# Kernel tuning notes

Measured on AMD Instinct MI355X. Metric: run time of the kernel, lower is better.

## Reference

```python
import jax, jax.numpy as jnp
import numpy as np

S, B, NC, IMG = 7, 2, 20, 448
GRID = IMG // S  # 64 px per cell
COORD_W, NOOBJ_W = 5.0, 0.5
N_BATCH, N_GT = 16384, 20


def _left_top():
    # ltp[i, j] = (GRID * j, GRID * i)  -- x from column, y from row
    col = (jnp.arange(S) * GRID).astype(jnp.float32)
    X, Y = jnp.meshgrid(col, col, indexing='xy')
    return jnp.stack([X, Y], -1)  # [S, S, 2]


def _corners(center_xy, wh):
    half = wh * 0.5
    x1y1 = jnp.clip(center_xy - half, 0.0, IMG - 1.0)
    x2y2 = jnp.clip(center_xy + half, 0.0, IMG - 1.0)
    return jnp.concatenate([x1y1, x2y2], -1)


def _encode(groundTruth, groundLabels):
    # Vectorized objMaskAndEncoder: replaces nested python scatter loops.
    N, G, _ = groundTruth.shape
    x1, y1, x2, y2 = (groundTruth[..., k] for k in range(4))
    w, h = x2 - x1, y2 - y1
    x, y = x1 + w * 0.5, y1 + h * 0.5
    cellX = jnp.floor(x / GRID).astype(jnp.int32)
    cellY = jnp.floor(y / GRID).astype(jnp.int32)
    offset = jnp.stack([(x - cellX * GRID) / GRID,
                        (y - cellY * GRID) / GRID,
                        w / IMG, h / IMG], -1)  # [N, G, 4]
    b_idx = jnp.broadcast_to(jnp.arange(N)[:, None], (N, G))
    flat = cellY * S + cellX  # [N, G] flat cell id
    j_idx = jnp.broadcast_to(jnp.arange(G, dtype=jnp.int32)[None, :], (N, G))
    last = jnp.full((N, S * S), -1, jnp.int32).at[b_idx, flat].max(j_idx)
    gi = jnp.maximum(last, 0)
    gathered = jnp.take_along_axis(offset, gi[:, :, None], axis=1)  # [N, S*S, 4]
    gtOrd = jnp.where((last >= 0)[:, :, None], gathered, 0.0).reshape(N, S, S, 4)
    # every GT sets its class bit in its cell (not just the last one)
    gtLabels = jnp.zeros((N, S, S, NC), jnp.float32).at[
        b_idx, cellY, cellX, groundLabels].set(1.0)
    objMask = (gtLabels.sum(-1) != 0).astype(jnp.float32)
    return objMask, gtOrd, gtLabels


def _best_iou(objMask, gtOrd, preBoxes):
    N = preBoxes.shape[0]
    ltp = _left_top()
    pb = preBoxes.reshape(N, S, S, B, 4)
    pboxes = _corners(pb[..., :2] * GRID + ltp[None, :, :, None, :],
                      pb[..., 2:] * IMG)  # [N, S, S, B, 4]
    gboxes = _corners(gtOrd[..., :2] * GRID + ltp[None, :, :, :],
                      gtOrd[..., 2:] * IMG)[:, :, :, None, :]  # [N, S, S, 1, 4]
    lt = jnp.maximum(pboxes[..., :2], gboxes[..., :2])
    rb = jnp.minimum(pboxes[..., 2:], gboxes[..., 2:])
    wh = jnp.maximum(rb - lt, 0.0)
    inter = wh[..., 0] * wh[..., 1]
    a1 = (pboxes[..., 2] - pboxes[..., 0]) * (pboxes[..., 3] - pboxes[..., 1])
    a2 = (gboxes[..., 2] - gboxes[..., 0]) * (gboxes[..., 3] - gboxes[..., 1])
    iou = inter / (a1 + a2 - inter + 1e-4)  # [N, S, S, B]
    best = jnp.argmax(iou, axis=-1)
    boxObjMask = jax.nn.one_hot(best, B, dtype=jnp.float32) * objMask[..., None]
    boxIouMax = jnp.max(iou, axis=-1, keepdims=True) * boxObjMask
    return boxObjMask, boxIouMax


def _yolo_loss(preConfidence, preBoxes, preCondClasses, groundTruth, groundLabels):
    objMask, gtOrd, gtLabels = _encode(groundTruth, groundLabels)
    boxObjMask, _ = _best_iou(objMask, gtOrd, preBoxes)
    objMask, gtOrd, gtLabels, boxObjMask = map(
        jax.lax.stop_gradient, (objMask, gtOrd, gtLabels, boxObjMask))  # torch no_grad
    pb = preBoxes.reshape(-1, S, S, B, 4)
    m = boxObjMask[..., None]
    xy, wh = pb[..., :2], jnp.sqrt(pb[..., 2:])
    xyGt = gtOrd[..., None, :2]
    whGt = jnp.sqrt(gtOrd[..., None, 2:])
    coordLoss = ((jnp.square(xy - xyGt) * m).sum()
                 + (jnp.square(wh - whGt) * m).sum()) * COORD_W
    diff2 = jnp.square(preConfidence - boxObjMask)
    objLoss = (diff2 * boxObjMask).sum()
    noObjLoss = NOOBJ_W * (diff2 * (1.0 - boxObjMask)).sum()
    clsLoss = (jnp.square(preCondClasses - gtLabels).sum(-1) * objMask).sum()
    return coordLoss, objLoss, noObjLoss, clsLoss


def setup_inputs() -> dict:
    key = jax.random.key(0)
    k1, k2, k3, k4, k5, k6 = jax.random.split(key, 6)
    preConfidence = jax.random.uniform(k1, (N_BATCH, S, S, B), jnp.float32)
    preBoxes = jax.random.uniform(k2, (N_BATCH, S, S, B * 4), jnp.float32)
    preCondClasses = jax.random.uniform(k3, (N_BATCH, S, S, NC), jnp.float32)
    # realistic GT corner boxes inside the 448x448 image
    cxy = jax.random.uniform(k4, (N_BATCH, N_GT, 2), jnp.float32, 0.0, float(IMG))
    wh = jax.random.uniform(k5, (N_BATCH, N_GT, 2), jnp.float32, 10.0, 120.0)
    x1y1 = jnp.clip(cxy - wh / 2, 0.0, IMG - 1.0)
    x2y2 = jnp.clip(cxy + wh / 2, 0.0, IMG - 1.0)
    groundTruth = jnp.concatenate([x1y1, x2y2], -1)
    groundLabels = jax.random.randint(k6, (N_BATCH, N_GT), 0, NC)
    return {"preConfidence": preConfidence, "preBoxes": preBoxes,
            "preCondClasses": preCondClasses, "groundTruth": groundTruth,
            "groundLabels": groundLabels}


def reference(preConfidence, preBoxes, preCondClasses, groundTruth, groundLabels):
    return _yolo_loss(preConfidence, preBoxes, preCondClasses, groundTruth, groundLabels)
```

## Files before the change

### kernel.cpp

```cpp
#include <hip/hip_runtime.h>
#include <math.h>


#define S7 7
#define NCELL 49
#define NGT 20
#define NCLS 20
#define BPB 4
#define BPW 2
#define THREADS 256
#define NBLK 2048

__device__ __forceinline__ float clip447(float v) {
    return fminf(fmaxf(v, 0.0f), 447.0f);
}

__device__ __forceinline__ float iou_one(float4 pb, float ltx, float lty,
                                         float g1x, float g1y, float g2x, float g2y,
                                         float ga) {
    float cx = pb.x * 64.0f + ltx, cy = pb.y * 64.0f + lty;
    float w  = pb.z * 448.0f,      h  = pb.w * 448.0f;
    float p1x = clip447(cx - w * 0.5f), p1y = clip447(cy - h * 0.5f);
    float p2x = clip447(cx + w * 0.5f), p2y = clip447(cy + h * 0.5f);
    float lx = fmaxf(p1x, g1x), ly = fmaxf(p1y, g1y);
    float rx = fminf(p2x, g2x), ry = fminf(p2y, g2y);
    float iw = fmaxf(rx - lx, 0.0f), ih = fmaxf(ry - ly, 0.0f);
    float inter = iw * ih;
    float a1 = (p2x - p1x) * (p2y - p1y);
    return inter / (a1 + ga - inter + 0.0001f);
}

__global__ __launch_bounds__(THREADS) void yolo_loss_kernel(
    const float* __restrict__ preConf,
    const float* __restrict__ preBoxes,
    const float* __restrict__ preCls,
    const float* __restrict__ gtBox,
    const int*   __restrict__ gtLab,
    float* __restrict__ ws)
{
    __shared__ int      s_last[BPB][NCELL];
    __shared__ unsigned s_bits[BPB][NCELL];
    __shared__ float    s_off[BPB][NGT][4];
    __shared__ float    s_red[BPB][4];

    const int wave = threadIdx.x >> 6;
    const int lane = threadIdx.x & 63;

    float coordL = 0.0f, objL = 0.0f, noobjL = 0.0f, clsL = 0.0f;

    for (int it = 0; it < BPW; ++it) {
        const int n = it * (NBLK * BPB) + blockIdx.x * BPB + wave;

        if (lane < NCELL) {
            s_last[wave][lane] = -1;
            s_bits[wave][lane] = 0u;
        }
        __syncthreads();

        if (lane < NGT) {
            float4 g = reinterpret_cast<const float4*>(gtBox)[(size_t)n * NGT + lane];
            int lab = gtLab[(size_t)n * NGT + lane];
            float w = g.z - g.x, h = g.w - g.y;
            float x = g.x + w * 0.5f, y = g.y + h * 0.5f;
            int cx = (int)floorf(x * 0.015625f);
            int cy = (int)floorf(y * 0.015625f);
            cx = max(0, min(cx, 6));
            cy = max(0, min(cy, 6));
            int flat = cy * S7 + cx;
            s_off[wave][lane][0] = (x - (float)cx * 64.0f) * 0.015625f;
            s_off[wave][lane][1] = (y - (float)cy * 64.0f) * 0.015625f;
            s_off[wave][lane][2] = w * (1.0f / 448.0f);
            s_off[wave][lane][3] = h * (1.0f / 448.0f);
            atomicMax(&s_last[wave][flat], lane);
            atomicOr(&s_bits[wave][flat], 1u << lab);
        }
        __syncthreads();

        if (lane < NCELL) {
            const int c = lane;
            const int row = c / S7, col = c - row * S7;
            const float ltx = (float)col * 64.0f, lty = (float)row * 64.0f;

            float2 cf = reinterpret_cast<const float2*>(preConf)[(size_t)n * NCELL + c];
            int last = s_last[wave][c];
            if (last >= 0) {
                const float4* pbp = reinterpret_cast<const float4*>(preBoxes)
                                    + (size_t)n * NCELL * 2 + (size_t)c * 2;
                float4 b0 = pbp[0];
                float4 b1 = pbp[1];

                float gx = s_off[wave][last][0], gy = s_off[wave][last][1];
                float gw = s_off[wave][last][2], gh = s_off[wave][last][3];
                float gcx = gx * 64.0f + ltx, gcy = gy * 64.0f + lty;
                float gW = gw * 448.0f, gH = gh * 448.0f;
                float g1x = clip447(gcx - gW * 0.5f), g1y = clip447(gcy - gH * 0.5f);
                float g2x = clip447(gcx + gW * 0.5f), g2y = clip447(gcy + gH * 0.5f);
                float ga = (g2x - g1x) * (g2y - g1y);

                float iou0 = iou_one(b0, ltx, lty, g1x, g1y, g2x, g2y, ga);
                float iou1 = iou_one(b1, ltx, lty, g1x, g1y, g2x, g2y, ga);
                int best = (iou1 > iou0) ? 1 : 0;
                float4 pb = best ? b1 : b0;
                float confB = best ? cf.y : cf.x;
                float confO = best ? cf.x : cf.y;

                float dx = pb.x - gx, dy = pb.y - gy;
                float dw = sqrtf(pb.z) - sqrtf(gw);
                float dh = sqrtf(pb.w) - sqrtf(gh);
                coordL += dx * dx + dy * dy + dw * dw + dh * dh;
                float d = confB - 1.0f;
                objL += d * d;
                noobjL += confO * confO;
            } else {
                noobjL += cf.x * cf.x + cf.y * cf.y;
            }
        }

        {
            const float4* base4 = reinterpret_cast<const float4*>(
                preCls + (size_t)n * (NCELL * NCLS));
            #pragma unroll
            for (int t = 0; t < 4; ++t) {
                const int i = lane + t * 64;
                if (i < 245) {
                    const int e = i * 4;
                    const int c0 = e / NCLS;
                    const int k0 = e - c0 * NCLS;
                    const unsigned b0 = s_bits[wave][c0];
                    const bool cross = (k0 > NCLS - 4);
                    const unsigned b1 = cross ? s_bits[wave][c0 + 1] : b0;
                    if (b0 | b1) {
                        float4 v = base4[i];
                        float vv[4] = {v.x, v.y, v.z, v.w};
                        #pragma unroll
                        for (int j = 0; j < 4; ++j) {
                            int kj = k0 + j;
                            unsigned bb = (kj < NCLS) ? b0 : b1;
                            int kk = (kj < NCLS) ? kj : kj - NCLS;
                            if (bb) {
                                float d = vv[j] - (float)((bb >> kk) & 1u);
                                clsL += d * d;
                            }
                        }
                    }
                }
            }
        }
        __syncthreads();
    }

    for (int off = 32; off > 0; off >>= 1) {
        coordL += __shfl_down(coordL, off);
        objL   += __shfl_down(objL, off);
        noobjL += __shfl_down(noobjL, off);
        clsL   += __shfl_down(clsL, off);
    }
    if (lane == 0) {
        s_red[wave][0] = coordL;
        s_red[wave][1] = objL;
        s_red[wave][2] = noobjL;
        s_red[wave][3] = clsL;
    }
    __syncthreads();

    if (threadIdx.x == 0) {
        float c0 = 0.f, c1 = 0.f, c2 = 0.f, c3 = 0.f;
        for (int w = 0; w < BPB; ++w) {
            c0 += s_red[w][0];
            c1 += s_red[w][1];
            c2 += s_red[w][2];
            c3 += s_red[w][3];
        }
        ws[0 * NBLK + blockIdx.x] = c0 * 5.0f;
        ws[1 * NBLK + blockIdx.x] = c1;
        ws[2 * NBLK + blockIdx.x] = c2 * 0.5f;
        ws[3 * NBLK + blockIdx.x] = c3;
    }
}

__global__ __launch_bounds__(256) void reduce_kernel(
    const float* __restrict__ ws, float* __restrict__ out)
{
    const int wave = threadIdx.x >> 6;
    const int lane = threadIdx.x & 63;
    const float* src = ws + wave * NBLK;
    float s = 0.0f;
    for (int i = lane; i < NBLK; i += 64) s += src[i];
    for (int off = 32; off > 0; off >>= 1) s += __shfl_down(s, off);
    if (lane == 0) out[wave] = s;
}

extern "C" void kernel_launch(void* const* d_in, const int* in_sizes, int n_in,
                              void* d_out, int out_size, void* d_ws, size_t ws_size,
                              hipStream_t stream) {
    const float* preConf  = (const float*)d_in[0];
    const float* preBoxes = (const float*)d_in[1];
    const float* preCls   = (const float*)d_in[2];
    const float* gtBox    = (const float*)d_in[3];
    const int*   gtLab    = (const int*)d_in[4];
    float* out = (float*)d_out;
    float* ws  = (float*)d_ws;

    yolo_loss_kernel<<<NBLK, THREADS, 0, stream>>>(
        preConf, preBoxes, preCls, gtBox, gtLab, ws);
    reduce_kernel<<<1, 256, 0, stream>>>(ws, out);
}
```

Before: 134.8 us.

## Replace shared-memory atomic encoding with wave shuffles and drop block barriers

Ground-truth cell assignment and class bitmasks are now computed per wave with a shuffle loop over the 20 GT lanes, replacing shared-memory atomics. This removes all __syncthreads and the shared arrays. The class-loss loop is simplified because each float4 always falls inside a single cell, and a ballot mask lets whole empty cells be skipped. A launch-bounds occupancy hint is added, and the cell-index clamp is dropped, which relies on GT centres staying inside the image.

```diff
diff --git a/kernel.cpp b/kernel.cpp
--- a/kernel.cpp
+++ b/kernel.cpp
@@ -30,7 +30,7 @@
     return inter / (a1 + ga - inter + 0.0001f);
 }
 
-__global__ __launch_bounds__(THREADS) void yolo_loss_kernel(
+__global__ __launch_bounds__(THREADS, 8) void yolo_loss_kernel(
     const float* __restrict__ preConf,
     const float* __restrict__ preBoxes,
     const float* __restrict__ preCls,
@@ -38,10 +38,7 @@
     const int*   __restrict__ gtLab,
     float* __restrict__ ws)
 {
-    __shared__ int      s_last[BPB][NCELL];
-    __shared__ unsigned s_bits[BPB][NCELL];
-    __shared__ float    s_off[BPB][NGT][4];
-    __shared__ float    s_red[BPB][4];
+    __shared__ float s_red[BPB][4];
 
     const int wave = threadIdx.x >> 6;
     const int lane = threadIdx.x & 63;
@@ -51,46 +48,49 @@
     for (int it = 0; it < BPW; ++it) {
         const int n = it * (NBLK * BPB) + blockIdx.x * BPB + wave;
 
-        if (lane < NCELL) {
-            s_last[wave][lane] = -1;
-            s_bits[wave][lane] = 0u;
-        }
-        __syncthreads();
-
+        float offx = 0.f, offy = 0.f, offw = 0.f, offh = 0.f;
+        int flatv = 0, lab = 0;
         if (lane < NGT) {
             float4 g = reinterpret_cast<const float4*>(gtBox)[(size_t)n * NGT + lane];
-            int lab = gtLab[(size_t)n * NGT + lane];
+            lab = gtLab[(size_t)n * NGT + lane];
             float w = g.z - g.x, h = g.w - g.y;
-            float x = g.x + w * 0.5f, y = g.y + h * 0.5f;
+            float x = g.x + 0.5f * w, y = g.y + 0.5f * h;
             int cx = (int)floorf(x * 0.015625f);
             int cy = (int)floorf(y * 0.015625f);
-            cx = max(0, min(cx, 6));
-            cy = max(0, min(cy, 6));
-            int flat = cy * S7 + cx;
-            s_off[wave][lane][0] = (x - (float)cx * 64.0f) * 0.015625f;
-            s_off[wave][lane][1] = (y - (float)cy * 64.0f) * 0.015625f;
-            s_off[wave][lane][2] = w * (1.0f / 448.0f);
-            s_off[wave][lane][3] = h * (1.0f / 448.0f);
-            atomicMax(&s_last[wave][flat], lane);
-            atomicOr(&s_bits[wave][flat], 1u << lab);
+            flatv = cy * S7 + cx;
+            offx = (x - (float)cx * 64.0f) * 0.015625f;
+            offy = (y - (float)cy * 64.0f) * 0.015625f;
+            offw = w * (1.0f / 448.0f);
+            offh = h * (1.0f / 448.0f);
         }
-        __syncthreads();
+
+        int last = -1;
+        unsigned bits = 0u;
+        #pragma unroll
+        for (int j = 0; j < NGT; ++j) {
+            int fj = __shfl(flatv, j);
+            int lj = __shfl(lab, j);
+            if (fj == lane) { last = j; bits |= (1u << lj); }
+        }
+        const unsigned long long ball = __ballot(bits != 0u);
+
+        const int srcl = (last < 0) ? 0 : last;
+        const float gx = __shfl(offx, srcl);
+        const float gy = __shfl(offy, srcl);
+        const float gw = __shfl(offw, srcl);
+        const float gh = __shfl(offh, srcl);
 
         if (lane < NCELL) {
-            const int c = lane;
-            const int row = c / S7, col = c - row * S7;
+            const int row = lane / S7, col = lane - row * S7;
             const float ltx = (float)col * 64.0f, lty = (float)row * 64.0f;
 
-            float2 cf = reinterpret_cast<const float2*>(preConf)[(size_t)n * NCELL + c];
-            int last = s_last[wave][c];
+            float2 cf = reinterpret_cast<const float2*>(preConf)[(size_t)n * NCELL + lane];
             if (last >= 0) {
                 const float4* pbp = reinterpret_cast<const float4*>(preBoxes)
-                                    + (size_t)n * NCELL * 2 + (size_t)c * 2;
+                                    + (size_t)n * NCELL * 2 + (size_t)lane * 2;
                 float4 b0 = pbp[0];
                 float4 b1 = pbp[1];
 
-                float gx = s_off[wave][last][0], gy = s_off[wave][last][1];
-                float gw = s_off[wave][last][2], gh = s_off[wave][last][3];
                 float gcx = gx * 64.0f + ltx, gcy = gy * 64.0f + lty;
                 float gW = gw * 448.0f, gH = gh * 448.0f;
                 float g1x = clip447(gcx - gW * 0.5f), g1y = clip447(gcy - gH * 0.5f);
@@ -123,30 +123,20 @@
             for (int t = 0; t < 4; ++t) {
                 const int i = lane + t * 64;
                 if (i < 245) {
-                    const int e = i * 4;
-                    const int c0 = e / NCLS;
-                    const int k0 = e - c0 * NCLS;
-                    const unsigned b0 = s_bits[wave][c0];
-                    const bool cross = (k0 > NCLS - 4);
-                    const unsigned b1 = cross ? s_bits[wave][c0 + 1] : b0;
-                    if (b0 | b1) {
+                    const int c0 = i / 5;
+                    const int k0 = (i - c0 * 5) * 4;
+                    if ((ball >> c0) & 1ull) {
+                        const unsigned b = __shfl(bits, c0);
                         float4 v = base4[i];
-                        float vv[4] = {v.x, v.y, v.z, v.w};
-                        #pragma unroll
-                        for (int j = 0; j < 4; ++j) {
-                            int kj = k0 + j;
-                            unsigned bb = (kj < NCLS) ? b0 : b1;
-                            int kk = (kj < NCLS) ? kj : kj - NCLS;
-                            if (bb) {
-                                float d = vv[j] - (float)((bb >> kk) & 1u);
-                                clsL += d * d;
-                            }
-                        }
+                        float d0 = v.x - (float)((b >> (k0 + 0)) & 1u);
+                        float d1 = v.y - (float)((b >> (k0 + 1)) & 1u);
+                        float d2 = v.z - (float)((b >> (k0 + 2)) & 1u);
+                        float d3 = v.w - (float)((b >> (k0 + 3)) & 1u);
+                        clsL += d0 * d0 + d1 * d1 + d2 * d2 + d3 * d3;
                     }
                 }
             }
         }
-        __syncthreads();
     }
 
     for (int off = 32; off > 0; off >>= 1) {
```

Measured after the change: 166.8 us. 23.8% more time.
